# Optimization experiments

Hardware: AMD Instinct MI355X
Metric: run time of the kernel (lower is better)

The kernel has to match this reference:

```python
import jax, jax.numpy as jnp
import numpy as np

IN_DIM, HIDDEN, OUT_DIM = 128, 64, 1
N_NODES_TOTAL = 200000  # 4 graphs x 50000 nodes
N_EDGES = 3200000
NUM_NODES_PER_GRAPH = 50000


def _glorot(key, shape):
    lim = float(np.sqrt(6.0 / (shape[0] + shape[1])))
    return jax.random.uniform(key, shape, jnp.float32, -lim, lim)


def setup_inputs() -> dict:
    key = jax.random.key(0)
    ks = jax.random.split(key, 32)
    inp = {
        "x": jax.random.normal(ks[0], (N_NODES_TOTAL, IN_DIM), jnp.float32),
        "edge_index": jax.random.randint(ks[1], (2, N_EDGES), 0, N_NODES_TOTAL, jnp.int32),
        "edge_weight": jax.random.uniform(ks[2], (N_EDGES,), jnp.float32),
        "edge_index2": jax.random.randint(ks[3], (2, N_EDGES), 0, N_NODES_TOTAL, jnp.int32),
        "edge_weight2": jax.random.uniform(ks[4], (N_EDGES,), jnp.float32),
        "num_nodes": NUM_NODES_PER_GRAPH,
    }
    dims = [(IN_DIM, HIDDEN), (HIDDEN, HIDDEN), (HIDDEN, OUT_DIM)]
    i = 5
    for b, (di, do) in zip(("ib1", "ib2", "ib3"), dims):
        for part in ("ln", "c1", "c2"):
            inp[f"{b}_{part}_w"] = _glorot(ks[i], (di, do)); i += 1
            inp[f"{b}_{part}_b"] = jnp.zeros((do,), jnp.float32)
    return inp


def digcn_conv(x, w, b, edge_index, edge_weight):
    # x' = x @ W; msg_e = edge_weight_e * x'[src_e]; out[dst] = sum msg; + bias
    xw = x @ w
    src, dst = edge_index[0], edge_index[1]
    msg = edge_weight[:, None] * xw[src]
    out = jax.ops.segment_sum(msg, dst, num_segments=x.shape[0])
    return out + b


def inception_block(x, ei, ew, ei2, ew2, lw, lb, c1w, c1b, c2w, c2b):
    x0 = x @ lw + lb
    x1 = digcn_conv(x, c1w, c1b, ei, ew)
    x2 = digcn_conv(x, c2w, c2b, ei2, ew2)
    return x0 + x1 + x2  # fusion='sum'; dropout is identity in eval mode


def reference(x, edge_index, edge_weight, edge_index2, edge_weight2, num_nodes,
              ib1_ln_w, ib1_ln_b, ib1_c1_w, ib1_c1_b, ib1_c2_w, ib1_c2_b,
              ib2_ln_w, ib2_ln_b, ib2_c1_w, ib2_c1_b, ib2_c2_w, ib2_c2_b,
              ib3_ln_w, ib3_ln_b, ib3_c1_w, ib3_c1_b, ib3_c2_w, ib3_c2_b):
    x = inception_block(x, edge_index, edge_weight, edge_index2, edge_weight2,
                        ib1_ln_w, ib1_ln_b, ib1_c1_w, ib1_c1_b, ib1_c2_w, ib1_c2_b)
    x = inception_block(x, edge_index, edge_weight, edge_index2, edge_weight2,
                        ib2_ln_w, ib2_ln_b, ib2_c1_w, ib2_c1_b, ib2_c2_w, ib2_c2_b)
    x = inception_block(x, edge_index, edge_weight, edge_index2, edge_weight2,
                        ib3_ln_w, ib3_ln_b, ib3_c1_w, ib3_c1_b, ib3_c2_w, ib3_c2_b)
    x_ = x.reshape(-1, num_nodes, OUT_DIM)
    out = jnp.max(x_, axis=1)  # readout='max'
    return (out, x, x)
```

## Files before the change

### kernel.cpp

```cpp
#include <hip/hip_runtime.h>
#include <hip/hip_bf16.h>

constexpr int NNODES = 200000;
constexpr int NGRAPH_NODES = 50000;
constexpr int NE = 3200000;
constexpr int H = 64;
constexpr int NBLK = (NNODES + 255) / 256;

template <int DI>
__global__ __launch_bounds__(256) void gemm3_kernel(
    const float* __restrict__ X,
    const float* __restrict__ Wl, const float* __restrict__ Bl,
    const float* __restrict__ W1, const float* __restrict__ B1,
    const float* __restrict__ W2, const float* __restrict__ B2,
    float* __restrict__ Y, float* __restrict__ S1, float* __restrict__ S2)
{
    __shared__ float xs[32][DI];
    const int tid = threadIdx.x;
    const int f = tid & 63;
    const int r = tid >> 6;
    const int base = blockIdx.x * 32;

    const float4* xg = reinterpret_cast<const float4*>(X + (size_t)base * DI);
    float4* xsv = reinterpret_cast<float4*>(&xs[0][0]);
    constexpr int NV = 32 * DI / 4;
    #pragma unroll
    for (int i = tid; i < NV; i += 256) xsv[i] = xg[i];
    __syncthreads();

    float accL[8], acc1[8], acc2[8];
    #pragma unroll
    for (int i = 0; i < 8; ++i) { accL[i] = 0.f; acc1[i] = 0.f; acc2[i] = 0.f; }

    for (int k = 0; k < DI; ++k) {
        float wl = Wl[k * H + f];
        float w1 = W1[k * H + f];
        float w2 = W2[k * H + f];
        #pragma unroll
        for (int i = 0; i < 8; ++i) {
            float xv = xs[r * 8 + i][k];
            accL[i] = fmaf(xv, wl, accL[i]);
            acc1[i] = fmaf(xv, w1, acc1[i]);
            acc2[i] = fmaf(xv, w2, acc2[i]);
        }
    }

    float bias = Bl[f] + B1[f] + B2[f];
    #pragma unroll
    for (int i = 0; i < 8; ++i) {
        size_t n = (size_t)(base + r * 8 + i);
        Y[n * H + f]  = accL[i] + bias;
        S1[n * H + f] = acc1[i];
        S2[n * H + f] = acc2[i];
    }
}

__global__ __launch_bounds__(256) void gemm3_out1_kernel(
    const float* __restrict__ X,
    const float* __restrict__ Wl, const float* __restrict__ Bl,
    const float* __restrict__ W1, const float* __restrict__ B1,
    const float* __restrict__ W2, const float* __restrict__ B2,
    float* __restrict__ Y, float* __restrict__ S1, float* __restrict__ S2)
{
    __shared__ float wls[64], w1s[64], w2s[64];
    const int tid = threadIdx.x;
    if (tid < 64) { wls[tid] = Wl[tid]; w1s[tid] = W1[tid]; w2s[tid] = W2[tid]; }
    __syncthreads();
    const int n = blockIdx.x * 256 + tid;
    if (n >= NNODES) return;
    const float4* xr = reinterpret_cast<const float4*>(X + (size_t)n * H);
    float aL = 0.f, a1 = 0.f, a2 = 0.f;
    #pragma unroll
    for (int kv = 0; kv < 16; ++kv) {
        float4 xv = xr[kv];
        int k = kv * 4;
        aL = fmaf(xv.x, wls[k + 0], aL); a1 = fmaf(xv.x, w1s[k + 0], a1); a2 = fmaf(xv.x, w2s[k + 0], a2);
        aL = fmaf(xv.y, wls[k + 1], aL); a1 = fmaf(xv.y, w1s[k + 1], a1); a2 = fmaf(xv.y, w2s[k + 1], a2);
        aL = fmaf(xv.z, wls[k + 2], aL); a1 = fmaf(xv.z, w1s[k + 2], a1); a2 = fmaf(xv.z, w2s[k + 2], a2);
        aL = fmaf(xv.w, wls[k + 3], aL); a1 = fmaf(xv.w, w1s[k + 3], a1); a2 = fmaf(xv.w, w2s[k + 3], a2);
    }
    float bias = Bl[0] + B1[0] + B2[0];
    Y[n] = aL + bias; S1[n] = a1; S2[n] = a2;
}

__global__ __launch_bounds__(256) void hist_full_kernel(
    const int* __restrict__ dst1, const int* __restrict__ dst2,
    int* __restrict__ cnt1, int* __restrict__ cnt2)
{
    const int* dst = blockIdx.y ? dst2 : dst1;
    int* cnt = blockIdx.y ? cnt2 : cnt1;
    const int t = blockIdx.x * 256 + threadIdx.x;
    const int tot = gridDim.x * 256;
    for (int e = t; e < NE; e += tot) atomicAdd(&cnt[dst[e]], 1);
}

__global__ __launch_bounds__(256) void scan_pass_a(
    int* __restrict__ cnt1, int* __restrict__ cnt2, int* __restrict__ bs)
{
    const int set = blockIdx.y;
    int* cnt = set ? cnt2 : cnt1;
    __shared__ int tmp[256];
    const int i = blockIdx.x * 256 + threadIdx.x;
    int v = (i < NNODES) ? cnt[i] : 0;
    tmp[threadIdx.x] = v;
    __syncthreads();
    #pragma unroll
    for (int off = 1; off < 256; off <<= 1) {
        int t = (threadIdx.x >= off) ? tmp[threadIdx.x - off] : 0;
        __syncthreads();
        tmp[threadIdx.x] += t;
        __syncthreads();
    }
    if (i < NNODES) cnt[i] = tmp[threadIdx.x] - v;
    if (threadIdx.x == 255) bs[set * NBLK + blockIdx.x] = tmp[255];
}

__global__ __launch_bounds__(1024) void scan_pass_b(
    int* __restrict__ bs, int* __restrict__ tot)
{
    __shared__ int tmp[1024];
    int* b = bs + blockIdx.x * NBLK;
    const int t = threadIdx.x;
    int v = (t < NBLK) ? b[t] : 0;
    tmp[t] = v;
    __syncthreads();
    for (int off = 1; off < 1024; off <<= 1) {
        int u = (t >= off) ? tmp[t - off] : 0;
        __syncthreads();
        tmp[t] += u;
        __syncthreads();
    }
    if (t < NBLK) b[t] = tmp[t] - v;
    if (t == 1023) tot[blockIdx.x] = tmp[1023];
}

__global__ __launch_bounds__(256) void scan_pass_c(
    const int* __restrict__ cnt1, const int* __restrict__ cnt2,
    const int* __restrict__ bs, const int* __restrict__ tot,
    int* __restrict__ rp1, int* __restrict__ rp2,
    int* __restrict__ cur1, int* __restrict__ cur2)
{
    const int set = blockIdx.y;
    const int* ex = set ? cnt2 : cnt1;
    int* rp = set ? rp2 : rp1;
    int* cur = set ? cur2 : cur1;
    const int off = bs[set * NBLK + blockIdx.x];
    const int i = blockIdx.x * 256 + threadIdx.x;
    if (i < NNODES) {
        int v = ex[i] + off;
        rp[i] = v;
        cur[i] = v;
    }
    if (blockIdx.x == 0 && threadIdx.x == 0) rp[NNODES] = tot[set];
}

__global__ __launch_bounds__(256) void place_kernel(
    const int* __restrict__ EI, const float* __restrict__ EW,
    int* __restrict__ cursor, uint2* __restrict__ sorted)
{
    const int t = blockIdx.x * 256 + threadIdx.x;
    const int tot = gridDim.x * 256;
    for (int e = t; e < NE; e += tot) {
        int s = EI[e];
        int d = EI[NE + e];
        int pos = atomicAdd(&cursor[d], 1);
        sorted[pos] = make_uint2((unsigned)s, __float_as_uint(EW[e]));
    }
}

__global__ __launch_bounds__(256) void csr_accum64_kernel(
    const uint2* __restrict__ E1, const int* __restrict__ rp1,
    const uint2* __restrict__ E2, const int* __restrict__ rp2,
    const float* __restrict__ S1, const float* __restrict__ S2,
    float* __restrict__ Y)
{
    const int lane = threadIdx.x & 63;
    const int wid = (blockIdx.x * 256 + threadIdx.x) >> 6;
    const int r0 = wid * 8;

    for (int r = r0; r < r0 + 8; ++r) {
        float acc = 0.f;
        {
            const int lo = rp1[r], hi = rp1[r + 1];
            int e = lo;
            for (; e + 4 <= hi; e += 4) {
                uint2 p0 = E1[e], p1 = E1[e + 1], p2 = E1[e + 2], p3 = E1[e + 3];
                float v0 = S1[(size_t)p0.x * H + lane];
                float v1 = S1[(size_t)p1.x * H + lane];
                float v2 = S1[(size_t)p2.x * H + lane];
                float v3 = S1[(size_t)p3.x * H + lane];
                acc = fmaf(__uint_as_float(p0.y), v0, acc);
                acc = fmaf(__uint_as_float(p1.y), v1, acc);
                acc = fmaf(__uint_as_float(p2.y), v2, acc);
                acc = fmaf(__uint_as_float(p3.y), v3, acc);
            }
            for (; e < hi; ++e) {
                uint2 p = E1[e];
                acc = fmaf(__uint_as_float(p.y), S1[(size_t)p.x * H + lane], acc);
            }
        }
        {
            const int lo = rp2[r], hi = rp2[r + 1];
            int e = lo;
            for (; e + 4 <= hi; e += 4) {
                uint2 p0 = E2[e], p1 = E2[e + 1], p2 = E2[e + 2], p3 = E2[e + 3];
                float v0 = S2[(size_t)p0.x * H + lane];
                float v1 = S2[(size_t)p1.x * H + lane];
                float v2 = S2[(size_t)p2.x * H + lane];
                float v3 = S2[(size_t)p3.x * H + lane];
                acc = fmaf(__uint_as_float(p0.y), v0, acc);
                acc = fmaf(__uint_as_float(p1.y), v1, acc);
                acc = fmaf(__uint_as_float(p2.y), v2, acc);
                acc = fmaf(__uint_as_float(p3.y), v3, acc);
            }
            for (; e < hi; ++e) {
                uint2 p = E2[e];
                acc = fmaf(__uint_as_float(p.y), S2[(size_t)p.x * H + lane], acc);
            }
        }
        Y[(size_t)r * H + lane] += acc;
    }
}

__device__ __forceinline__ unsigned fkey(float v) {
    unsigned u = __float_as_uint(v);
    return (u & 0x80000000u) ? ~u : (u | 0x80000000u);
}

__global__ __launch_bounds__(256) void csr_accum1_readout_kernel(
    const uint2* __restrict__ E1, const int* __restrict__ rp1,
    const uint2* __restrict__ E2, const int* __restrict__ rp2,
    const float* __restrict__ s1, const float* __restrict__ s2,
    const float* __restrict__ Y3,
    float* __restrict__ body1, float* __restrict__ body2,
    unsigned int* __restrict__ keys)
{
    __shared__ unsigned int smax[4];
    const int tid = threadIdx.x;
    if (tid < 4) smax[tid] = 0u;
    __syncthreads();
    const int r = blockIdx.x * 256 + tid;
    if (r < NNODES) {
        float acc = Y3[r];
        for (int e = rp1[r]; e < rp1[r + 1]; ++e) {
            uint2 p = E1[e];
            acc = fmaf(__uint_as_float(p.y), s1[p.x], acc);
        }
        for (int e = rp2[r]; e < rp2[r + 1]; ++e) {
            uint2 p = E2[e];
            acc = fmaf(__uint_as_float(p.y), s2[p.x], acc);
        }
        body1[r] = acc;
        body2[r] = acc;
        atomicMax(&smax[r / NGRAPH_NODES], fkey(acc));
    }
    __syncthreads();
    if (tid < 4 && smax[tid]) atomicMax(&keys[tid], smax[tid]);
}

__global__ void finalize_kernel(const unsigned int* __restrict__ keys,
                                float* __restrict__ out)
{
    int i = threadIdx.x;
    if (i < 4) {
        unsigned k = keys[i];
        unsigned u = (k & 0x80000000u) ? (k ^ 0x80000000u) : ~k;
        out[i] = __uint_as_float(u);
    }
}

__global__ __launch_bounds__(256) void scatter64_kernel(
    const int* __restrict__ EI, const float* __restrict__ EW,
    const float* __restrict__ S, float* __restrict__ Y)
{
    const int lane = threadIdx.x & 63;
    const int wid = (blockIdx.x * 256 + threadIdx.x) >> 6;
    const int nw = (gridDim.x * 256) >> 6;
    for (int e = wid; e < NE; e += nw) {
        int s = EI[e];
        int d = EI[NE + e];
        float w = EW[e];
        float v = S[(size_t)s * H + lane];
        unsafeAtomicAdd(&Y[(size_t)d * H + lane], w * v);
    }
}

__global__ __launch_bounds__(256) void scatter1_kernel(
    const int* __restrict__ EI, const float* __restrict__ EW,
    const float* __restrict__ S, float* __restrict__ Y)
{
    const int t = blockIdx.x * 256 + threadIdx.x;
    const int tot = gridDim.x * 256;
    for (int e = t; e < NE; e += tot) {
        int s = EI[e];
        int d = EI[NE + e];
        float w = EW[e];
        unsafeAtomicAdd(&Y[d], w * S[s]);
    }
}

__global__ __launch_bounds__(256) void readout_kernel(
    const float* __restrict__ Y3, float* __restrict__ body1,
    float* __restrict__ body2, unsigned int* __restrict__ keys)
{
    __shared__ unsigned int smax[4];
    const int tid = threadIdx.x;
    if (tid < 4) smax[tid] = 0u;
    __syncthreads();
    const int i = blockIdx.x * 256 + tid;
    if (i < NNODES) {
        float v = Y3[i];
        body1[i] = v;
        body2[i] = v;
        atomicMax(&smax[i / NGRAPH_NODES], fkey(v));
    }
    __syncthreads();
    if (tid < 4 && smax[tid]) atomicMax(&keys[tid], smax[tid]);
}

extern "C" void kernel_launch(void* const* d_in, const int* in_sizes, int n_in,
                              void* d_out, int out_size, void* d_ws, size_t ws_size,
                              hipStream_t stream)
{
    const float* x   = (const float*)d_in[0];
    const int*   ei  = (const int*)d_in[1];
    const float* ew  = (const float*)d_in[2];
    const int*   ei2 = (const int*)d_in[3];
    const float* ew2 = (const float*)d_in[4];
    const float* W[18];
    for (int i = 0; i < 18; ++i) W[i] = (const float*)d_in[6 + i];

    float* Y  = (float*)d_ws;
    float* S1 = Y + (size_t)NNODES * H;
    float* S2 = S1 + (size_t)NNODES * H;
    float* Y3 = S2 + (size_t)NNODES * H;
    uint2* E1 = (uint2*)(Y3 + NNODES);
    uint2* E2 = E1 + NE;
    unsigned int* keys = (unsigned int*)(E2 + NE);
    int* cnt1 = (int*)(keys + 4);
    int* cnt2 = cnt1 + NNODES;
    int* rp1  = cnt2 + NNODES;
    int* rp2  = rp1 + NNODES + 1;
    int* cur1 = rp2 + NNODES + 1;
    int* cur2 = cur1 + NNODES;
    int* bs   = cur2 + NNODES;
    int* tot  = bs + 2 * NBLK;
    size_t needed = (size_t)((char*)(tot + 2) - (char*)d_ws);

    float* out = (float*)d_out;

    if (ws_size >= needed) {
        hipMemsetAsync(keys, 0, (size_t)(4 + 2 * NNODES) * sizeof(int), stream);

        hist_full_kernel<<<dim3(1024, 2), 256, 0, stream>>>(ei + NE, ei2 + NE, cnt1, cnt2);
        scan_pass_a<<<dim3(NBLK, 2), 256, 0, stream>>>(cnt1, cnt2, bs);
        scan_pass_b<<<2, 1024, 0, stream>>>(bs, tot);
        scan_pass_c<<<dim3(NBLK, 2), 256, 0, stream>>>(cnt1, cnt2, bs, tot,
                                                       rp1, rp2, cur1, cur2);
        place_kernel<<<2048, 256, 0, stream>>>(ei,  ew,  cur1, E1);
        place_kernel<<<2048, 256, 0, stream>>>(ei2, ew2, cur2, E2);

        gemm3_kernel<128><<<NNODES / 32, 256, 0, stream>>>(
            x, W[0], W[1], W[2], W[3], W[4], W[5], Y, S1, S2);
        csr_accum64_kernel<<<6250, 256, 0, stream>>>(E1, rp1, E2, rp2, S1, S2, Y);

        gemm3_kernel<64><<<NNODES / 32, 256, 0, stream>>>(
            Y, W[6], W[7], W[8], W[9], W[10], W[11], Y, S1, S2);
        csr_accum64_kernel<<<6250, 256, 0, stream>>>(E1, rp1, E2, rp2, S1, S2, Y);

        gemm3_out1_kernel<<<(NNODES + 255) / 256, 256, 0, stream>>>(
            Y, W[12], W[13], W[14], W[15], W[16], W[17], Y3, S1, S2);
        csr_accum1_readout_kernel<<<(NNODES + 255) / 256, 256, 0, stream>>>(
            E1, rp1, E2, rp2, S1, S2, Y3, out + 4, out + 4 + NNODES, keys);
        finalize_kernel<<<1, 64, 0, stream>>>(keys, out);
    } else {
        unsigned int* okeys = (unsigned int*)(Y3 + NNODES);
        hipMemsetAsync(okeys, 0, 4 * sizeof(unsigned int), stream);

        gemm3_kernel<128><<<NNODES / 32, 256, 0, stream>>>(
            x, W[0], W[1], W[2], W[3], W[4], W[5], Y, S1, S2);
        scatter64_kernel<<<2048, 256, 0, stream>>>(ei,  ew,  S1, Y);
        scatter64_kernel<<<2048, 256, 0, stream>>>(ei2, ew2, S2, Y);

        gemm3_kernel<64><<<NNODES / 32, 256, 0, stream>>>(
            Y, W[6], W[7], W[8], W[9], W[10], W[11], Y, S1, S2);
        scatter64_kernel<<<2048, 256, 0, stream>>>(ei,  ew,  S1, Y);
        scatter64_kernel<<<2048, 256, 0, stream>>>(ei2, ew2, S2, Y);

        gemm3_out1_kernel<<<(NNODES + 255) / 256, 256, 0, stream>>>(
            Y, W[12], W[13], W[14], W[15], W[16], W[17], Y3, S1, S2);
        scatter1_kernel<<<2048, 256, 0, stream>>>(ei,  ew,  S1, Y3);
        scatter1_kernel<<<2048, 256, 0, stream>>>(ei2, ew2, S2, Y3);

        readout_kernel<<<(NNODES + 255) / 256, 256, 0, stream>>>(
            Y3, out + 4, out + 4 + NNODES, okeys);
        finalize_kernel<<<1, 64, 0, stream>>>(okeys, out);
    }
}
```

Measured before the change: 1.956 ms.

## Store gathered conv features in fp16 and batch CSR gather loads

The per-node transformed features S1/S2 that the CSR aggregation gathers are now written and read as fp16, which halves the bytes of the dominant random gather traffic. The aggregation kernel also preloads its row pointers into registers and unrolls the edge loop by 8 so more gathers are in flight at once. The histogram kernel reads destination indices as int4, and the two place launches are merged into one 2D grid. The cost is reduced precision in the messages, which may move outputs past tolerance, plus higher register pressure from the wider unroll.

```diff
diff --git a/kernel.cpp b/kernel.cpp
--- a/kernel.cpp
+++ b/kernel.cpp
@@ -1,5 +1,6 @@
 #include <hip/hip_runtime.h>
 #include <hip/hip_bf16.h>
+#include <hip/hip_fp16.h>
 
 constexpr int NNODES = 200000;
 constexpr int NGRAPH_NODES = 50000;
@@ -7,13 +8,13 @@
 constexpr int H = 64;
 constexpr int NBLK = (NNODES + 255) / 256;
 
-template <int DI>
+template <int DI, typename TS>
 __global__ __launch_bounds__(256) void gemm3_kernel(
     const float* __restrict__ X,
     const float* __restrict__ Wl, const float* __restrict__ Bl,
     const float* __restrict__ W1, const float* __restrict__ B1,
     const float* __restrict__ W2, const float* __restrict__ B2,
-    float* __restrict__ Y, float* __restrict__ S1, float* __restrict__ S2)
+    float* __restrict__ Y, TS* __restrict__ S1, TS* __restrict__ S2)
 {
     __shared__ float xs[32][DI];
     const int tid = threadIdx.x;
@@ -50,8 +51,8 @@
     for (int i = 0; i < 8; ++i) {
         size_t n = (size_t)(base + r * 8 + i);
         Y[n * H + f]  = accL[i] + bias;
-        S1[n * H + f] = acc1[i];
-        S2[n * H + f] = acc2[i];
+        S1[n * H + f] = (TS)acc1[i];
+        S2[n * H + f] = (TS)acc2[i];
     }
 }
 
@@ -91,7 +92,14 @@
     int* cnt = blockIdx.y ? cnt2 : cnt1;
     const int t = blockIdx.x * 256 + threadIdx.x;
     const int tot = gridDim.x * 256;
-    for (int e = t; e < NE; e += tot) atomicAdd(&cnt[dst[e]], 1);
+    const int4* d4 = reinterpret_cast<const int4*>(dst);
+    for (int q = t; q < NE / 4; q += tot) {
+        int4 v = d4[q];
+        atomicAdd(&cnt[v.x], 1);
+        atomicAdd(&cnt[v.y], 1);
+        atomicAdd(&cnt[v.z], 1);
+        atomicAdd(&cnt[v.w], 1);
+    }
 }
 
 __global__ __launch_bounds__(256) void scan_pass_a(
@@ -155,9 +163,16 @@
 }
 
 __global__ __launch_bounds__(256) void place_kernel(
-    const int* __restrict__ EI, const float* __restrict__ EW,
-    int* __restrict__ cursor, uint2* __restrict__ sorted)
-{
+    const int* __restrict__ ei1, const float* __restrict__ ew1,
+    const int* __restrict__ ei2, const float* __restrict__ ew2,
+    int* __restrict__ cur1, int* __restrict__ cur2,
+    uint2* __restrict__ sorted1, uint2* __restrict__ sorted2)
+{
+    const int set = blockIdx.y;
+    const int* EI = set ? ei2 : ei1;
+    const float* EW = set ? ew2 : ew1;
+    int* cursor = set ? cur2 : cur1;
+    uint2* sorted = set ? sorted2 : sorted1;
     const int t = blockIdx.x * 256 + threadIdx.x;
     const int tot = gridDim.x * 256;
     for (int e = t; e < NE; e += tot) {
@@ -171,54 +186,65 @@
 __global__ __launch_bounds__(256) void csr_accum64_kernel(
     const uint2* __restrict__ E1, const int* __restrict__ rp1,
     const uint2* __restrict__ E2, const int* __restrict__ rp2,
-    const float* __restrict__ S1, const float* __restrict__ S2,
+    const __half* __restrict__ S1, const __half* __restrict__ S2,
     float* __restrict__ Y)
 {
     const int lane = threadIdx.x & 63;
     const int wid = (blockIdx.x * 256 + threadIdx.x) >> 6;
     const int r0 = wid * 8;
 
-    for (int r = r0; r < r0 + 8; ++r) {
+    int b1[9], b2[9];
+    #pragma unroll
+    for (int i = 0; i < 9; ++i) b1[i] = rp1[r0 + i];
+    #pragma unroll
+    for (int i = 0; i < 9; ++i) b2[i] = rp2[r0 + i];
+
+    #pragma unroll 1
+    for (int r = 0; r < 8; ++r) {
         float acc = 0.f;
         {
-            const int lo = rp1[r], hi = rp1[r + 1];
-            int e = lo;
-            for (; e + 4 <= hi; e += 4) {
-                uint2 p0 = E1[e], p1 = E1[e + 1], p2 = E1[e + 2], p3 = E1[e + 3];
-                float v0 = S1[(size_t)p0.x * H + lane];
-                float v1 = S1[(size_t)p1.x * H + lane];
-                float v2 = S1[(size_t)p2.x * H + lane];
-                float v3 = S1[(size_t)p3.x * H + lane];
-                acc = fmaf(__uint_as_float(p0.y), v0, acc);
-                acc = fmaf(__uint_as_float(p1.y), v1, acc);
-                acc = fmaf(__uint_as_float(p2.y), v2, acc);
-                acc = fmaf(__uint_as_float(p3.y), v3, acc);
+            int e = b1[r];
+            const int hi = b1[r + 1];
+            for (; e + 8 <= hi; e += 8) {
+                uint2 p[8];
+                float v[8];
+                #pragma unroll
+                for (int j = 0; j < 8; ++j) p[j] = E1[e + j];
+                #pragma unroll
+                for (int j = 0; j < 8; ++j)
+                    v[j] = __half2float(S1[(size_t)p[j].x * H + lane]);
+                #pragma unroll
+                for (int j = 0; j < 8; ++j)
+                    acc = fmaf(__uint_as_float(p[j].y), v[j], acc);
             }
             for (; e < hi; ++e) {
                 uint2 p = E1[e];
-                acc = fmaf(__uint_as_float(p.y), S1[(size_t)p.x * H + lane], acc);
+                acc = fmaf(__uint_as_float(p.y),
+                           __half2float(S1[(size_t)p.x * H + lane]), acc);
             }
         }
         {
-            const int lo = rp2[r], hi = rp2[r + 1];
-            int e = lo;
-            for (; e + 4 <= hi; e += 4) {
-                uint2 p0 = E2[e], p1 = E2[e + 1], p2 = E2[e + 2], p3 = E2[e + 3];
-                float v0 = S2[(size_t)p0.x * H + lane];
-                float v1 = S2[(size_t)p1.x * H + lane];
-                float v2 = S2[(size_t)p2.x * H + lane];
-                float v3 = S2[(size_t)p3.x * H + lane];
-                acc = fmaf(__uint_as_float(p0.y), v0, acc);
-                acc = fmaf(__uint_as_float(p1.y), v1, acc);
-                acc = fmaf(__uint_as_float(p2.y), v2, acc);
-                acc = fmaf(__uint_as_float(p3.y), v3, acc);
+            int e = b2[r];
+            const int hi = b2[r + 1];
+            for (; e + 8 <= hi; e += 8) {
+                uint2 p[8];
+                float v[8];
+                #pragma unroll
+                for (int j = 0; j < 8; ++j) p[j] = E2[e + j];
+                #pragma unroll
+                for (int j = 0; j < 8; ++j)
+                    v[j] = __half2float(S2[(size_t)p[j].x * H + lane]);
+                #pragma unroll
+                for (int j = 0; j < 8; ++j)
+                    acc = fmaf(__uint_as_float(p[j].y), v[j], acc);
             }
             for (; e < hi; ++e) {
                 uint2 p = E2[e];
-                acc = fmaf(__uint_as_float(p.y), S2[(size_t)p.x * H + lane], acc);
+                acc = fmaf(__uint_as_float(p.y),
+                           __half2float(S2[(size_t)p.x * H + lane]), acc);
             }
         }
-        Y[(size_t)r * H + lane] += acc;
+        Y[(size_t)(r0 + r) * H + lane] += acc;
     }
 }
 
@@ -347,6 +373,9 @@
     int* tot  = bs + 2 * NBLK;
     size_t needed = (size_t)((char*)(tot + 2) - (char*)d_ws);
 
+    __half* hS1 = (__half*)S1;
+    __half* hS2 = (__half*)S2;
+
     float* out = (float*)d_out;
 
     if (ws_size >= needed) {
@@ -357,16 +386,16 @@
         scan_pass_b<<<2, 1024, 0, stream>>>(bs, tot);
         scan_pass_c<<<dim3(NBLK, 2), 256, 0, stream>>>(cnt1, cnt2, bs, tot,
                                                        rp1, rp2, cur1, cur2);
-        place_kernel<<<2048, 256, 0, stream>>>(ei,  ew,  cur1, E1);
-        place_kernel<<<2048, 256, 0, stream>>>(ei2, ew2, cur2, E2);
-
-        gemm3_kernel<128><<<NNODES / 32, 256, 0, stream>>>(
-            x, W[0], W[1], W[2], W[3], W[4], W[5], Y, S1, S2);
-        csr_accum64_kernel<<<6250, 256, 0, stream>>>(E1, rp1, E2, rp2, S1, S2, Y);
-
-        gemm3_kernel<64><<<NNODES / 32, 256, 0, stream>>>(
-            Y, W[6], W[7], W[8], W[9], W[10], W[11], Y, S1, S2);
-        csr_accum64_kernel<<<6250, 256, 0, stream>>>(E1, rp1, E2, rp2, S1, S2, Y);
+        place_kernel<<<dim3(2048, 2), 256, 0, stream>>>(ei, ew, ei2, ew2,
+                                                        cur1, cur2, E1, E2);
+
+        gemm3_kernel<128, __half><<<NNODES / 32, 256, 0, stream>>>(
+            x, W[0], W[1], W[2], W[3], W[4], W[5], Y, hS1, hS2);
+        csr_accum64_kernel<<<6250, 256, 0, stream>>>(E1, rp1, E2, rp2, hS1, hS2, Y);
+
+        gemm3_kernel<64, __half><<<NNODES / 32, 256, 0, stream>>>(
+            Y, W[6], W[7], W[8], W[9], W[10], W[11], Y, hS1, hS2);
+        csr_accum64_kernel<<<6250, 256, 0, stream>>>(E1, rp1, E2, rp2, hS1, hS2, Y);
 
         gemm3_out1_kernel<<<(NNODES + 255) / 256, 256, 0, stream>>>(
             Y, W[12], W[13], W[14], W[15], W[16], W[17], Y3, S1, S2);
@@ -377,12 +406,12 @@
         unsigned int* okeys = (unsigned int*)(Y3 + NNODES);
         hipMemsetAsync(okeys, 0, 4 * sizeof(unsigned int), stream);
 
-        gemm3_kernel<128><<<NNODES / 32, 256, 0, stream>>>(
+        gemm3_kernel<128, float><<<NNODES / 32, 256, 0, stream>>>(
             x, W[0], W[1], W[2], W[3], W[4], W[5], Y, S1, S2);
         scatter64_kernel<<<2048, 256, 0, stream>>>(ei,  ew,  S1, Y);
         scatter64_kernel<<<2048, 256, 0, stream>>>(ei2, ew2, S2, Y);
 
-        gemm3_kernel<64><<<NNODES / 32, 256, 0, stream>>>(
+        gemm3_kernel<64, float><<<NNODES / 32, 256, 0, stream>>>(
             Y, W[6], W[7], W[8], W[9], W[10], W[11], Y, S1, S2);
         scatter64_kernel<<<2048, 256, 0, stream>>>(ei,  ew,  S1, Y);
         scatter64_kernel<<<2048, 256, 0, stream>>>(ei2, ew2, S2, Y);
```

Measured after the change: 1.817 ms. 1.08x faster.
